# Optimization experiments

Hardware: AMD Instinct MI355X
Metric: run time of the kernel (lower is better)

The kernel has to match this reference:

```python
import jax, jax.numpy as jnp
import numpy as np
import math

D_MODEL = 1024
N_HEADS = 16
FACTOR = 5


def setup_inputs() -> dict:
    key = jax.random.key(0)
    ks = jax.random.split(key, 8)
    B, L, S, d = 8, 4096, 4096, D_MODEL
    sc = 1.0 / math.sqrt(d)
    perm = jnp.asarray(np.random.default_rng(0).permutation(L), jnp.int32)
    return {
        "queries": jax.random.normal(ks[0], (B, L, d), jnp.float32),
        "keys": jax.random.normal(ks[1], (B, S, d), jnp.float32),
        "values": jax.random.normal(ks[2], (B, S, d), jnp.float32),
        "perm": perm,
        "Wq": jax.random.normal(ks[3], (d, d), jnp.float32) * sc,
        "bq": jnp.zeros((d,), jnp.float32),
        "Wk": jax.random.normal(ks[4], (d, d), jnp.float32) * sc,
        "bk": jnp.zeros((d,), jnp.float32),
        "Wv": jax.random.normal(ks[5], (d, d), jnp.float32) * sc,
        "bv": jnp.zeros((d,), jnp.float32),
        "Wo": jax.random.normal(ks[6], (d, d), jnp.float32) * sc,
        "bo": jnp.zeros((d,), jnp.float32),
    }


def reference(queries, keys, values, perm, Wq, bq, Wk, bk, Wv, bv, Wo, bo):
    B, L, d = queries.shape
    S = keys.shape[1]
    H = N_HEADS
    dk = d // H

    q = (queries @ Wq + bq).reshape(B, L, H, dk)
    k = (keys @ Wk + bk).reshape(B, S, H, dk)
    v = (values @ Wv + bv).reshape(B, S, H, dk)

    # ProbSparse: u = min(factor * ceil(log(S)), L)  (static, shape-derived)
    u_part = FACTOR * int(math.ceil(math.log(S)))
    u = min(u_part, L)

    # sample u queries (perm replaces torch.randperm for determinism)
    q_sample = q[:, perm[:u]]                                   # [B,u,H,dk]
    scores_sample = jnp.einsum('buhd,bshd->bhus', q_sample, k)  # [B,H,u,S]

    # sparsity measurement M = max_s - mean_s
    M = scores_sample.max(-1) - scores_sample.sum(-1) / S       # [B,H,u]
    _, M_top = jax.lax.top_k(M, u)                              # [B,H,u] indices in [0,u)

    # gather top-u queries per (batch, head) along the L axis
    qT = q.transpose(0, 2, 1, 3)                                # [B,H,L,dk]
    q_red = jnp.take_along_axis(qT, M_top[..., None], axis=2)   # [B,H,u,dk]

    scores = jnp.einsum('bhud,bshd->bhus', q_red, k)            # [B,H,u,S]
    attn = jax.nn.softmax(scores, axis=-1)
    context = jnp.einsum('bhus,bshd->buhd', attn, v).reshape(B, u, d)
    output = context @ Wo + bo                                  # [B,u,d]
    return output, attn
```

## Files before the change

kernel.cpp:

```cpp
#include <hip/hip_runtime.h>
#include <stdint.h>
#include <stddef.h>

#define DEV static __device__ __forceinline__

typedef short short8 __attribute__((ext_vector_type(8)));
typedef short short4v __attribute__((ext_vector_type(4)));
typedef float f32x4 __attribute__((ext_vector_type(4)));
typedef _Float16 half8 __attribute__((ext_vector_type(8)));

DEV uint16_t f2h(float x){
  union { _Float16 h; uint16_t u; } c; c.h = (_Float16)x; return c.u;
}

DEV f32x4 mfma16h(short8 a, short8 b, f32x4 c){
  union { short8 s; half8 h; } ua, ub; ua.s = a; ub.s = b;
  return __builtin_amdgcn_mfma_f32_16x16x32_f16(ua.h, ub.h, c, 0, 0, 0);
}

typedef const __attribute__((address_space(1))) void* gas1;
typedef __attribute__((address_space(3))) void* las3;
DEV void async16(const void* g, void* l){
  __builtin_amdgcn_global_load_lds((gas1)g, (las3)l, 16, 0, 0);
}

DEV int swzoct(int row, int oct){ return (oct & ~7) | ((oct ^ row) & 7); }
DEV short8 lds_frag(const short* base, int row, int rowOcts, int oct){
  int o = swzoct(row, oct);
  return *(const short8*)(base + row * rowOcts * 8 + o * 8);
}
DEV void lds_store8(short* base, int row, int rowOcts, int oct, short8 v){
  int o = swzoct(row, oct);
  *(short8*)(base + row * rowOcts * 8 + o * 8) = v;
}

__global__ __launch_bounds__(256) void pa_prep_weights(
    const float* __restrict__ Wk, const float* __restrict__ Wv,
    uint16_t* WkT, uint16_t* WvT){
  int which = blockIdx.y;
  const float* W = which ? Wv : Wk;
  uint16_t* O = which ? WvT : WkT;
  int e0 = (blockIdx.x * 256 + threadIdx.x) * 4;
  #pragma unroll
  for(int c=0;c<4;c++){
    int e = e0 + c; int n = e >> 10, k = e & 1023;
    O[e] = f2h(W[(size_t)k*1024 + n]);
  }
}

__global__ __launch_bounds__(256) void pa_prep_inputs(
    const float* __restrict__ keys, const float* __restrict__ values,
    uint16_t* __restrict__ kf, uint16_t* __restrict__ vf){
  size_t e = ((size_t)blockIdx.x * 256 + threadIdx.x) * 8;
  const float* src = blockIdx.y ? values : keys;
  uint16_t* dst = blockIdx.y ? vf : kf;
  float4 u0 = *(const float4*)(src + e);
  float4 u1 = *(const float4*)(src + e + 4);
  float xs[8] = {u0.x,u0.y,u0.z,u0.w,u1.x,u1.y,u1.z,u1.w};
  short8 hv;
  #pragma unroll
  for(int c=0;c<8;c++) hv[c] = (short)f2h(xs[c]);
  *(short8*)(dst + e) = hv;
}

__global__ __launch_bounds__(256) void pa_q_stage1(
    const float* __restrict__ queries, const int* __restrict__ perm,
    const float* __restrict__ Wq, double* __restrict__ qpart){
  __shared__ alignas(16) float Alds[96*32];
  __shared__ alignas(16) float Blds[32*128];
  int ct = blockIdx.x, kc = blockIdx.y, b = blockIdx.z;
  int t = threadIdx.x;
  int tr = t >> 4, tc = t & 15;
  const float* qb = queries + (size_t)b*4096*1024;
  const float* srcA[3];
  #pragma unroll
  for(int rr=0; rr<3; rr++){
    int chunk = rr*256 + t;
    int row = chunk >> 3, c8 = chunk & 7;
    int rid = (row < 45) ? perm[row] : (row < 90 ? row - 45 : 0);
    srcA[rr] = qb + (size_t)rid*1024 + c8*4;
  }
  const float* srcB[4];
  #pragma unroll
  for(int rr=0; rr<4; rr++){
    int chunk = rr*256 + t;
    int kk = chunk >> 5, c = chunk & 31;
    srcB[rr] = Wq + (size_t)kk*1024 + ct*128 + c*4;
  }
  double acc[6][8];
  #pragma unroll
  for(int i=0;i<6;i++)
    #pragma unroll
    for(int jj=0;jj<8;jj++) acc[i][jj] = 0.0;
  int k0 = kc*128;
  for(int ks=0; ks<4; ks++){
    int kk0 = k0 + ks*32;
    #pragma unroll
    for(int rr=0; rr<3; rr++)
      async16(srcA[rr] + kk0, (char*)Alds + (rr*256 + t)*16);
    #pragma unroll
    for(int rr=0; rr<4; rr++)
      async16(srcB[rr] + (size_t)kk0*1024, (char*)Blds + (rr*256 + t)*16);
    __syncthreads();
    #pragma unroll
    for(int kk=0; kk<32; kk++){
      double av[6];
      #pragma unroll
      for(int i=0;i<6;i++) av[i] = (double)Alds[(tr*6+i)*32 + kk];
      float4 b0 = *(const float4*)(Blds + kk*128 + tc*8);
      float4 b1 = *(const float4*)(Blds + kk*128 + tc*8 + 4);
      double bv[8] = {(double)b0.x,(double)b0.y,(double)b0.z,(double)b0.w,
                      (double)b1.x,(double)b1.y,(double)b1.z,(double)b1.w};
      #pragma unroll
      for(int i=0;i<6;i++)
        #pragma unroll
        for(int jj=0;jj<8;jj++)
          acc[i][jj] += av[i]*bv[jj];
    }
    __syncthreads();
  }
  #pragma unroll
  for(int i=0;i<6;i++){
    int r = tr*6 + i;
    double* dst = qpart + (((size_t)b*96 + r)*8 + kc)*1024 + ct*128 + tc*8;
    #pragma unroll
    for(int jj=0;jj<8;jj++) dst[jj] = acc[i][jj];
  }
}

__global__ __launch_bounds__(256) void pa_q_finalize(
    const double* __restrict__ qpart, const float* __restrict__ bq,
    float* q_f32, uint16_t* q_f16){
  int slot = blockIdx.x, b = blockIdx.y;
  int j = (slot < 45) ? slot : ((slot >= 48 && slot < 93) ? (45 + slot - 48) : -1);
  #pragma unroll
  for(int c=0;c<4;c++){
    int n = threadIdx.x * 4 + c;
    float v = 0.f;
    if(j >= 0){
      const double* p = qpart + (((size_t)b*96 + j)*8)*1024 + n;
      double s = 0.0;
      #pragma unroll
      for(int kc=0;kc<8;kc++) s += p[(size_t)kc*1024];
      v = (float)(s + (double)bq[n]);
    }
    int h = n >> 6, d = n & 63;
    size_t idx = (((size_t)(b*16 + h))*96 + slot)*64 + d;
    q_f32[idx] = v;
    q_f16[idx] = f2h(v);
  }
}

template<bool TR>
__global__ __launch_bounds__(256) void pa_kv_gemm(
    const uint16_t* __restrict__ Ag, const uint16_t* __restrict__ Bg,
    const float* __restrict__ bias, uint16_t* __restrict__ out){
  __shared__ alignas(16) short Ah[128*64], Bh[128*64];
  int tid = threadIdx.x, wid = tid >> 6, lane = tid & 63;
  int bid = blockIdx.x;
  int xcd = bid & 7, slot = bid >> 3;
  int mt = xcd*32 + (slot >> 3), nt = slot & 7;
  int m0 = mt*128, n0 = nt*128;
  int rsub = lane >> 3;
  int soct = (lane & 7) ^ rsub;
  const uint16_t* a0 = Ag + (size_t)(m0 + wid*32 + rsub)*1024 + soct*8;
  const uint16_t* b0 = Bg + (size_t)(n0 + wid*32 + rsub)*1024 + soct*8;
  short* lA = Ah + wid*32*64;
  short* lB = Bh + wid*32*64;
  f32x4 acc[4][4];
  #pragma unroll
  for(int i=0;i<4;i++)
    #pragma unroll
    for(int jj=0;jj<4;jj++) acc[i][jj] = (f32x4){0.f,0.f,0.f,0.f};
  int wr = wid >> 1, wc = wid & 1;
  for(int kb=0; kb<16; kb++){
    int ko = kb*64;
    #pragma unroll
    for(int q=0;q<4;q++){
      async16(a0 + ko + q*8*1024, lA + q*512);
      async16(b0 + ko + q*8*1024, lB + q*512);
    }
    __syncthreads();
    short8 Af[4][2];
    #pragma unroll
    for(int mf=0;mf<4;mf++)
      #pragma unroll
      for(int k2=0;k2<2;k2++){
        int row = wr*64 + mf*16 + (lane & 15);
        int oct = k2*4 + (lane >> 4);
        Af[mf][k2] = lds_frag(Ah, row, 8, oct);
      }
    #pragma unroll
    for(int nf=0;nf<4;nf++){
      short8 Bf[2];
      #pragma unroll
      for(int k2=0;k2<2;k2++){
        int row = wc*64 + nf*16 + (lane & 15);
        int oct = k2*4 + (lane >> 4);
        Bf[k2] = lds_frag(Bh, row, 8, oct);
      }
      #pragma unroll
      for(int mf=0;mf<4;mf++)
        #pragma unroll
        for(int k2=0;k2<2;k2++)
          acc[mf][nf] = mfma16h(Af[mf][k2], Bf[k2], acc[mf][nf]);
    }
    __syncthreads();
  }
  int b = m0 >> 12, s_base = m0 & 4095;
  #pragma unroll
  for(int mf=0;mf<4;mf++)
    #pragma unroll
    for(int nf=0;nf<4;nf++){
      int srow = s_base + wr*64 + mf*16 + ((lane >> 4) << 2);
      int ncol = n0 + wc*64 + nf*16 + (lane & 15);
      float bia = bias[ncol];
      int h = ncol >> 6, d = ncol & 63;
      if constexpr(!TR){
        size_t base = ((((size_t)(b*16 + h))*4096 + srow)*64 + d);
        #pragma unroll
        for(int i=0;i<4;i++)
          out[base + (size_t)i*64] = f2h(acc[mf][nf][i] + bia);
      } else {
        short4v pk;
        #pragma unroll
        for(int i=0;i<4;i++) pk[i] = (short)f2h(acc[mf][nf][i] + bia);
        *(short4v*)(out + ((((size_t)(b*16 + h))*64 + d)*4096 + srow)) = pk;
      }
    }
}

__global__ __launch_bounds__(256) void pa_p1_stats(
    const uint16_t* __restrict__ q_f16, const uint16_t* __restrict__ khg,
    float* __restrict__ stats){
  __shared__ alignas(16) short qf[96*64], kh[128*64];
  int chunk = blockIdx.x, h = blockIdx.y, b = blockIdx.z;
  int tid = threadIdx.x, wid = tid >> 6, lane = tid & 63;
  const uint16_t* qsf = q_f16 + ((size_t)(b*16 + h))*96*64;
  #pragma unroll
  for(int jj=0;jj<3;jj++){
    int oc = tid*3 + jj;
    int sl = oc >> 3, o = oc & 7;
    lds_store8(qf, sl, 8, o, *(const short8*)(qsf + sl*64 + o*8));
  }
  float t1v[3][4], t2v[3][4], t3v[3][4], ssum[3][4], mm[3][4], zz[3][4];
  int t1i[3][4], t2i[3][4], t3i[3][4];
  #pragma unroll
  for(int a=0;a<3;a++)
    #pragma unroll
    for(int i=0;i<4;i++){
      t1v[a][i]=-3e38f; t2v[a][i]=-3e38f; t3v[a][i]=-3e38f; ssum[a][i]=0.f;
      mm[a][i]=-3e38f; zz[a][i]=0.f; t1i[a][i]=0; t2i[a][i]=0; t3i[a][i]=0;
    }
  int rsub = lane >> 3, soct = (lane & 7) ^ rsub;
  const uint16_t* khb = khg + (((size_t)(b*16 + h))*4096)*64;
  __syncthreads();
  for(int st=0; st<4; st++){
    int sg0 = chunk*512 + st*128;
    #pragma unroll
    for(int q=0;q<4;q++){
      int row = wid*32 + q*8;
      async16(khb + (size_t)(sg0 + row + rsub)*64 + soct*8, kh + row*64);
    }
    __syncthreads();
    short8 Bf[2][2];
    #pragma unroll
    for(int nf=0;nf<2;nf++)
      #pragma unroll
      for(int k2=0;k2<2;k2++){
        int scol = wid*32 + nf*16 + (lane & 15);
        int oct = k2*4 + (lane >> 4);
        Bf[nf][k2] = lds_frag(kh, scol, 8, oct);
      }
    #pragma unroll
    for(int mf=0;mf<6;mf++){
      short8 af[2];
      #pragma unroll
      for(int k2=0;k2<2;k2++){
        int row = mf*16 + (lane & 15);
        int oct = k2*4 + (lane >> 4);
        af[k2] = lds_frag(qf, row, 8, oct);
      }
      f32x4 a0 = (f32x4){0.f,0.f,0.f,0.f}, a1 = a0;
      #pragma unroll
      for(int k2=0;k2<2;k2++){
        a0 = mfma16h(af[k2], Bf[0][k2], a0);
        a1 = mfma16h(af[k2], Bf[1][k2], a1);
      }
      #pragma unroll
      for(int nf=0;nf<2;nf++){
        int sgl = sg0 + wid*32 + nf*16 + (lane & 15);
        #pragma unroll
        for(int i=0;i<4;i++){
          float v = nf ? a1[i] : a0[i];
          if(mf < 3){
            ssum[mf][i] += v;
            if(v > t1v[mf][i]){
              t3v[mf][i]=t2v[mf][i]; t3i[mf][i]=t2i[mf][i];
              t2v[mf][i]=t1v[mf][i]; t2i[mf][i]=t1i[mf][i];
              t1v[mf][i]=v; t1i[mf][i]=sgl;
            } else if(v > t2v[mf][i]){
              t3v[mf][i]=t2v[mf][i]; t3i[mf][i]=t2i[mf][i];
              t2v[mf][i]=v; t2i[mf][i]=sgl;
            } else if(v > t3v[mf][i]){
              t3v[mf][i]=v; t3i[mf][i]=sgl;
            }
          } else {
            int q = mf - 3;
            float mn = fmaxf(mm[q][i], v);
            zz[q][i] = zz[q][i]*__expf(mm[q][i]-mn) + __expf(v-mn);
            mm[q][i] = mn;
          }
        }
      }
    }
    __syncthreads();
  }
  size_t sbase = (((((size_t)b*16 + h)*8 + chunk)*4 + wid)*96)*8;
  #pragma unroll
  for(int mf=0;mf<3;mf++)
    #pragma unroll
    for(int i=0;i<4;i++){
      float v1=t1v[mf][i], v2=t2v[mf][i], v3=t3v[mf][i], sm=ssum[mf][i];
      int i1=t1i[mf][i], i2=t2i[mf][i], i3=t3i[mf][i];
      #pragma unroll
      for(int msk=1; msk<16; msk<<=1){
        float w1=__shfl_xor(v1,msk,64), w2=__shfl_xor(v2,msk,64), w3=__shfl_xor(v3,msk,64);
        int j1=__shfl_xor(i1,msk,64), j2=__shfl_xor(i2,msk,64), j3=__shfl_xor(i3,msk,64);
        sm += __shfl_xor(sm,msk,64);
        if(w1 > v1){
          float tv; int ti;
          tv=v1; v1=w1; w1=tv; ti=i1; i1=j1; j1=ti;
          tv=v2; v2=w2; w2=tv; ti=i2; i2=j2; j2=ti;
          tv=v3; v3=w3; w3=tv; ti=i3; i3=j3; j3=ti;
        }
        if(w1 > v2){
          v3=v2; i3=i2; v2=w1; i2=j1;
          if(w2 > v3){ v3=w2; i3=j2; }
        } else if(w1 > v3){ v3=w1; i3=j1; }
      }
      if((lane & 15) == 0){
        int sl = mf*16 + ((lane >> 4) << 2) + i;
        float* dst = stats + sbase + (size_t)sl*8;
        dst[0]=v1; dst[1]=__int_as_float(i1); dst[2]=v2; dst[3]=__int_as_float(i2);
        dst[4]=v3; dst[5]=__int_as_float(i3); dst[6]=sm;
      }
    }
  #pragma unroll
  for(int q=0;q<3;q++)
    #pragma unroll
    for(int i=0;i<4;i++){
      float m1=mm[q][i], z1=zz[q][i];
      #pragma unroll
      for(int msk=1; msk<16; msk<<=1){
        float m2=__shfl_xor(m1,msk,64), z2=__shfl_xor(z1,msk,64);
        float mn = fmaxf(m1,m2);
        z1 = z1*__expf(m1-mn) + z2*__expf(m2-mn);
        m1 = mn;
      }
      if((lane & 15) == 0){
        int sl = 48 + q*16 + ((lane >> 4) << 2) + i;
        float* dst = stats + sbase + (size_t)sl*8;
        dst[0]=m1; dst[1]=z1;
      }
    }
}

__global__ __launch_bounds__(256) void pa_sort_mark(
    const float* __restrict__ stats,
    float* __restrict__ mzfin,
    float* __restrict__ Mv_g, float* __restrict__ Ssum_g,
    int* __restrict__ mlist_g, int* __restrict__ clist_g,
    int* __restrict__ nmark_g){
  int h = blockIdx.x, b = blockIdx.y;
  int bh = b*16 + h;
  __shared__ float Mv[48], Ssum[48];
  __shared__ int I1[48], I2[48], I3[48];
  __shared__ int order[48], mlist[48], flags[48];
  __shared__ int clist[144];
  __shared__ int nmark;
  int t = threadIdx.x;
  const float* sb = stats + (((size_t)bh)*8*4*96)*8;
  if(t < 48) flags[t] = 0;
  if(t < 48){
    float v1=-3e38f, v2=-3e38f, v3=-3e38f, sm=0.f; int i1=0, i2=0, i3=0;
    for(int c=0;c<8;c++)
      for(int w=0;w<4;w++){
        const float* p = sb + (((size_t)c*4 + w)*96 + t)*8;
        float w1=p[0], w2=p[2], w3=p[4];
        int j1=__float_as_int(p[1]), j2=__float_as_int(p[3]), j3=__float_as_int(p[5]);
        sm += p[6];
        if(w1 > v1){
          float tv; int ti;
          tv=v1; v1=w1; w1=tv; ti=i1; i1=j1; j1=ti;
          tv=v2; v2=w2; w2=tv; ti=i2; i2=j2; j2=ti;
          tv=v3; v3=w3; w3=tv; ti=i3; i3=j3; j3=ti;
        }
        if(w1 > v2){
          v3=v2; i3=i2; v2=w1; i2=j1;
          if(w2 > v3){ v3=w2; i3=j2; }
        } else if(w1 > v3){ v3=w1; i3=j1; }
      }
    Mv[t] = v1 - sm*(1.0f/4096.0f);
    I1[t]=i1; I2[t]=i2; I3[t]=i3; Ssum[t]=sm;
  }
  if(t >= 64 && t < 112){
    int i = t - 64;
    float m1=-3e38f, z1=0.f;
    for(int c=0;c<8;c++)
      for(int w=0;w<4;w++){
        const float* p = sb + (((size_t)c*4 + w)*96 + 48 + i)*8;
        float m2=p[0], z2=p[1];
        float mn = fmaxf(m1,m2);
        z1 = z1*__expf(m1-mn) + z2*__expf(m2-mn);
        m1 = mn;
      }
    mzfin[((size_t)bh*48 + i)*2 + 0] = m1;
    mzfin[((size_t)bh*48 + i)*2 + 1] = z1;
  }
  __syncthreads();
  if(t < 64){
    float v = (t < 45) ? Mv[t] : -3e38f;
    int rank = 0;
    #pragma unroll
    for(int j=0;j<45;j++){
      float vj = __shfl(v, j, 64);
      rank += (vj > v) || (vj == v && j < (int)t);
    }
    if(t < 45) order[rank] = t;
  }
  __syncthreads();
  if(t < 44){
    if(Mv[order[t]] - Mv[order[t+1]] < 0.025f){
      flags[order[t]] = 1; flags[order[t+1]] = 1;
    }
  }
  __syncthreads();
  if(t == 0){
    int cnt=0;
    for(int i=0;i<45;i++) if(flags[i]){
      clist[3*cnt]   = I1[i];
      clist[3*cnt+1] = I2[i];
      clist[3*cnt+2] = I3[i];
      mlist[cnt++]=i;
    }
    nmark = cnt;
  }
  __syncthreads();
  int nm = nmark;
  if(t < 48){
    Mv_g[(size_t)bh*48 + t] = Mv[t];
    Ssum_g[(size_t)bh*48 + t] = Ssum[t];
  }
  if(t < nm) mlist_g[(size_t)bh*48 + t] = mlist[t];
  if(t < 3*nm) clist_g[(size_t)bh*144 + t] = clist[t];
  if(t == 0) nmark_g[bh] = nm;
}

__global__ __launch_bounds__(256) void pa_refine(
    const float* __restrict__ keys, const float* __restrict__ Wk,
    const float* __restrict__ q_f32,
    const int* __restrict__ mlist_g, const int* __restrict__ clist_g,
    const int* __restrict__ nmark_g, double* __restrict__ scx_g){
  int cid = blockIdx.x, h = blockIdx.y, b = blockIdx.z;
  int bh = b*16 + h;
  int nc = nmark_g[bh]*3;
  if(cid >= nc) return;
  __shared__ double red[256];
  int t = threadIdx.x;
  int kq = t >> 6, d = t & 63;
  int sidx = clist_g[(size_t)bh*144 + cid];
  int u = mlist_g[(size_t)bh*48 + cid/3];
  const float* krow = keys + ((size_t)b*4096 + sidx)*1024;
  double acc = 0.0;
  int col = h*64 + d;
  #pragma unroll 8
  for(int k=kq*256; k<kq*256+256; k++)
    acc += (double)krow[k] * (double)Wk[(size_t)k*1024 + col];
  red[t] = acc;
  __syncthreads();
  if(t < 64){
    double kd = red[t] + red[64+t] + red[128+t] + red[192+t];
    double sp = kd * (double)q_f32[((size_t)bh*96 + u)*64 + t];
    #pragma unroll
    for(int m=1; m<64; m<<=1) sp += __shfl_xor(sp, m, 64);
    if(t == 0) scx_g[(size_t)bh*144 + cid] = sp;
  }
}

__global__ __launch_bounds__(64) void pa_final_rank(
    const float* __restrict__ Mv_g, const float* __restrict__ Ssum_g,
    const int* __restrict__ mlist_g, const int* __restrict__ nmark_g,
    const double* __restrict__ scx_g, int* __restrict__ invrk){
  int h = blockIdx.x, b = blockIdx.y;
  int bh = b*16 + h;
  __shared__ float Mv[48];
  int t = threadIdx.x;
  if(t < 48) Mv[t] = Mv_g[(size_t)bh*48 + t];
  int nm = nmark_g[bh];
  __syncthreads();
  if(t < nm){
    int u = mlist_g[(size_t)bh*48 + t];
    const double* s3 = scx_g + (size_t)bh*144 + 3*t;
    double mx = s3[0];
    if(s3[1] > mx) mx = s3[1];
    if(s3[2] > mx) mx = s3[2];
    Mv[u] = (float)mx - Ssum_g[(size_t)bh*48 + u]*(1.0f/4096.0f);
  }
  __syncthreads();
  float v = (t < 45) ? Mv[t] : -3e38f;
  int rank = 0;
  #pragma unroll
  for(int j=0;j<45;j++){
    float vj = __shfl(v, j, 64);
    rank += (vj > v) || (vj == v && j < (int)t);
  }
  if(t < 45) invrk[(size_t)bh*48 + t] = rank;
}

__global__ __launch_bounds__(256) void pa_p2_attn(
    const uint16_t* __restrict__ q_f16, const uint16_t* __restrict__ khg,
    const uint16_t* __restrict__ v_t,
    const float* __restrict__ mzfin, const int* __restrict__ invrk,
    float* __restrict__ attn_out, float* __restrict__ ctx2){
  __shared__ alignas(16) short qf[48*64];
  __shared__ alignas(16) short kh[64*64];
  __shared__ alignas(16) short vT[64*64];
  __shared__ alignas(16) short Pl[48*64];
  int chunk = blockIdx.x, h = blockIdx.y, b = blockIdx.z;
  int tid = threadIdx.x, wid = tid >> 6, lane = tid & 63;
  const uint16_t* qsf = q_f16 + (((size_t)(b*16 + h))*96 + 48)*64;
  for(int oc=tid; oc<384; oc+=256){
    int sl = oc >> 3, o = oc & 7;
    lds_store8(qf, sl, 8, o, *(const short8*)(qsf + sl*64 + o*8));
  }
  float mreg[3][4], invz[3][4];
  int rrk[3][4];
  #pragma unroll
  for(int mf=0;mf<3;mf++)
    #pragma unroll
    for(int i=0;i<4;i++){
      int u = mf*16 + ((lane >> 4) << 2) + i;
      mreg[mf][i] = mzfin[(((size_t)(b*16 + h))*48 + u)*2 + 0];
      invz[mf][i] = 1.f / mzfin[(((size_t)(b*16 + h))*48 + u)*2 + 1];
      rrk[mf][i] = invrk[((size_t)(b*16 + h))*48 + u];
    }
  f32x4 ctx[3];
  #pragma unroll
  for(int mf=0;mf<3;mf++) ctx[mf] = (f32x4){0.f,0.f,0.f,0.f};
  int rsub = lane >> 3, soct = (lane & 7) ^ rsub;
  const uint16_t* khb = khg + (((size_t)(b*16 + h))*4096)*64;
  const uint16_t* vtb = v_t + (((size_t)(b*16 + h))*64)*4096;
  __syncthreads();
  for(int st=0; st<8; st++){
    int sg0 = chunk*512 + st*64;
    #pragma unroll
    for(int q=0;q<2;q++){
      int row = wid*16 + q*8;
      async16(khb + (size_t)(sg0 + row + rsub)*64 + soct*8, kh + row*64);
      async16(vtb + (size_t)(row + rsub)*4096 + sg0 + soct*8, vT + row*64);
    }
    __syncthreads();
    short8 Bf[2];
    #pragma unroll
    for(int k2=0;k2<2;k2++){
      int scol = wid*16 + (lane & 15);
      int oct = k2*4 + (lane >> 4);
      Bf[k2] = lds_frag(kh, scol, 8, oct);
    }
    #pragma unroll
    for(int mf=0;mf<3;mf++){
      short8 af[2];
      #pragma unroll
      for(int k2=0;k2<2;k2++){
        int row = mf*16 + (lane & 15);
        int oct = k2*4 + (lane >> 4);
        af[k2] = lds_frag(qf, row, 8, oct);
      }
      f32x4 a0 = (f32x4){0.f,0.f,0.f,0.f};
      #pragma unroll
      for(int k2=0;k2<2;k2++)
        a0 = mfma16h(af[k2], Bf[k2], a0);
      int scl = wid*16 + (lane & 15);
      #pragma unroll
      for(int i=0;i<4;i++){
        int u = mf*16 + ((lane >> 4) << 2) + i;
        float p = __expf(a0[i] - mreg[mf][i]) * invz[mf][i];
        if(u < 45){
          attn_out[(((size_t)(b*16 + h))*45 + rrk[mf][i])*4096 + sg0 + scl] = p;
        }
        int oct = scl >> 3;
        int o = (oct ^ (u & 7)) & 7;
        Pl[u*64 + o*8 + (scl & 7)] = (short)f2h(p);
      }
    }
    __syncthreads();
    #pragma unroll
    for(int k2=0;k2<2;k2++){
      int oct = k2*4 + (lane >> 4);
      int drow = wid*16 + (lane & 15);
      short8 bv = lds_frag(vT, drow, 8, oct);
      #pragma unroll
      for(int mf=0;mf<3;mf++){
        int row = mf*16 + (lane & 15);
        short8 ap = lds_frag(Pl, row, 8, oct);
        ctx[mf] = mfma16h(ap, bv, ctx[mf]);
      }
    }
    __syncthreads();
  }
  #pragma unroll
  for(int mf=0;mf<3;mf++)
    #pragma unroll
    for(int i=0;i<4;i++){
      int u = mf*16 + ((lane >> 4) << 2) + i;
      if(u < 45){
        int d = wid*16 + (lane & 15);
        ctx2[(((size_t)chunk*8 + b)*45 + rrk[mf][i])*1024 + h*64 + d] = ctx[mf][i];
      }
    }
}

__global__ __launch_bounds__(256) void pa_out_gemm(
    const float* __restrict__ ctx2, const float* __restrict__ Wo,
    const float* __restrict__ bo, float* __restrict__ out){
  __shared__ float cl[8][1024];
  int bx = blockIdx.x, by = blockIdx.y;
  int t = threadIdx.x;
  for(int e=t; e<8*1024; e+=256){
    int rr = e >> 10, k = e & 1023;
    size_t grow = (size_t)by*8 + rr;
    float s = 0.f;
    #pragma unroll
    for(int c=0;c<8;c++) s += ctx2[((size_t)c*360 + grow)*1024 + k];
    cl[rr][k] = s;
  }
  __syncthreads();
  int quad = t & 63, rg = t >> 6;
  int n = bx*256 + quad*4;
  float acc[2][4];
  #pragma unroll
  for(int rr=0;rr<2;rr++)
    #pragma unroll
    for(int c=0;c<4;c++) acc[rr][c]=0.f;
  for(int k=0;k<1024;k++){
    float4 w = *(const float4*)(Wo + (size_t)k*1024 + n);
    float c0 = cl[rg*2][k], c1 = cl[rg*2+1][k];
    acc[0][0] += c0*w.x; acc[0][1] += c0*w.y; acc[0][2] += c0*w.z; acc[0][3] += c0*w.w;
    acc[1][0] += c1*w.x; acc[1][1] += c1*w.y; acc[1][2] += c1*w.z; acc[1][3] += c1*w.w;
  }
  #pragma unroll
  for(int rr=0;rr<2;rr++){
    size_t grow = (size_t)by*8 + rg*2 + rr;
    #pragma unroll
    for(int c=0;c<4;c++) out[grow*1024 + n + c] = acc[rr][c] + bo[n + c];
  }
}

extern "C" void kernel_launch(void* const* d_in, const int* in_sizes, int n_in,
                              void* d_out, int out_size, void* d_ws, size_t ws_size,
                              hipStream_t stream){
  const float* queries = (const float*)d_in[0];
  const float* keys    = (const float*)d_in[1];
  const float* values  = (const float*)d_in[2];
  const int*   perm    = (const int*)d_in[3];
  const float* Wq = (const float*)d_in[4]; const float* bq = (const float*)d_in[5];
  const float* Wk = (const float*)d_in[6]; const float* bk = (const float*)d_in[7];
  const float* Wv = (const float*)d_in[8]; const float* bv = (const float*)d_in[9];
  const float* Wo = (const float*)d_in[10]; const float* bo = (const float*)d_in[11];

  char* ws = (char*)d_ws;
  const size_t SZ = (size_t)33554432;
  uint16_t* kf_in = (uint16_t*)(ws);
  uint16_t* vf_in = (uint16_t*)(ws + SZ*2);
  uint16_t* k_o   = (uint16_t*)(ws + SZ*4);
  uint16_t* WkT   = (uint16_t*)(ws + SZ*6);
  uint16_t* WvT   = (uint16_t*)(ws + SZ*6 + 2097152);
  float*    q_f32 = (float*)   (ws + SZ*6 + 4194304);
  uint16_t* q_f16 = (uint16_t*)(ws + SZ*6 + 7340032);

  char* rg = ws + SZ*2;
  double* qpart   = (double*)rg;
  float*  stats   = (float*)rg;
  float*  mzfin   = (float*)(rg + 12582912);
  int*    invrk   = (int*)  (rg + 12632064);
  float*  ctx2    = (float*)(rg + 12656640);
  float*  Mv_g    = (float*)(rg + 24453120);
  float*  Ssum_g  = (float*)(rg + 24477696);
  int*    mlist_g = (int*)  (rg + 24502272);
  int*    clist_g = (int*)  (rg + 24526848);
  int*    nmark_g = (int*)  (rg + 24600576);
  double* scx_g   = (double*)(rg + 24601088);
  uint16_t* v_t = kf_in;

  float* out  = (float*)d_out;
  float* attn = out + (size_t)360*1024;

  pa_prep_weights<<<dim3(1024,2), 256, 0, stream>>>(Wk, Wv, WkT, WvT);
  pa_q_stage1<<<dim3(8,8,8), 256, 0, stream>>>(queries, perm, Wq, qpart);
  pa_q_finalize<<<dim3(96,8), 256, 0, stream>>>(qpart, bq, q_f32, q_f16);
  pa_prep_inputs<<<dim3(16384,2), 256, 0, stream>>>(keys, values, kf_in, vf_in);
  pa_kv_gemm<false><<<2048, 256, 0, stream>>>(kf_in, WkT, bk, k_o);
  pa_kv_gemm<true><<<2048, 256, 0, stream>>>(vf_in, WvT, bv, v_t);
  pa_p1_stats<<<dim3(8,16,8), 256, 0, stream>>>(q_f16, k_o, stats);
  pa_sort_mark<<<dim3(16,8), 256, 0, stream>>>(stats, mzfin, Mv_g, Ssum_g, mlist_g, clist_g, nmark_g);
  pa_refine<<<dim3(135,16,8), 256, 0, stream>>>(keys, Wk, q_f32, mlist_g, clist_g, nmark_g, scx_g);
  pa_final_rank<<<dim3(16,8), 64, 0, stream>>>(Mv_g, Ssum_g, mlist_g, nmark_g, scx_g, invrk);
  pa_p2_attn<<<dim3(8,16,8), 256, 0, stream>>>(q_f16, k_o, v_t, mzfin, invrk, attn, ctx2);
  pa_out_gemm<<<dim3(4,45), 256, 0, stream>>>(ctx2, Wo, bo, out);
}
```

Before: 636.8 us.

## Merge K and V projection GEMMs into one launch with 128-wide K tiles

The two templated K and V projection GEMM launches become one kernel with a 2D grid, where blockIdx.y picks K or V operands, so both projections run concurrently. The K-step tile grows from 64 to 128, halving loop iterations and barriers per block while doubling LDS use to 64 KB per block. v_t now gets its own workspace buffer instead of aliasing kf_in, which removes the write-after-read hazard between the two GEMMs but enlarges the workspace. The larger LDS footprint may lower occupancy, and the bool template becomes a runtime branch.

```diff
diff --git a/kernel.cpp b/kernel.cpp
--- a/kernel.cpp
+++ b/kernel.cpp
@@ -151,58 +151,63 @@
   }
 }
 
-template<bool TR>
 __global__ __launch_bounds__(256) void pa_kv_gemm(
-    const uint16_t* __restrict__ Ag, const uint16_t* __restrict__ Bg,
-    const float* __restrict__ bias, uint16_t* __restrict__ out){
-  __shared__ alignas(16) short Ah[128*64], Bh[128*64];
+    const uint16_t* __restrict__ kfA, const uint16_t* __restrict__ vfA,
+    const uint16_t* __restrict__ WkB, const uint16_t* __restrict__ WvB,
+    const float* __restrict__ bk, const float* __restrict__ bv,
+    uint16_t* __restrict__ k_o, uint16_t* __restrict__ v_t){
+  __shared__ alignas(16) short Ah[128*128], Bh[128*128];
+  const bool TR = (blockIdx.y == 1);
+  const uint16_t* Ag = TR ? vfA : kfA;
+  const uint16_t* Bg = TR ? WvB : WkB;
+  const float* bias = TR ? bv : bk;
   int tid = threadIdx.x, wid = tid >> 6, lane = tid & 63;
   int bid = blockIdx.x;
   int xcd = bid & 7, slot = bid >> 3;
   int mt = xcd*32 + (slot >> 3), nt = slot & 7;
   int m0 = mt*128, n0 = nt*128;
-  int rsub = lane >> 3;
-  int soct = (lane & 7) ^ rsub;
-  const uint16_t* a0 = Ag + (size_t)(m0 + wid*32 + rsub)*1024 + soct*8;
-  const uint16_t* b0 = Bg + (size_t)(n0 + wid*32 + rsub)*1024 + soct*8;
-  short* lA = Ah + wid*32*64;
-  short* lB = Bh + wid*32*64;
+  int rsub = lane >> 4;
+  int l15 = lane & 15;
+  short* lA = Ah + wid*32*128;
+  short* lB = Bh + wid*32*128;
   f32x4 acc[4][4];
   #pragma unroll
   for(int i=0;i<4;i++)
     #pragma unroll
     for(int jj=0;jj<4;jj++) acc[i][jj] = (f32x4){0.f,0.f,0.f,0.f};
   int wr = wid >> 1, wc = wid & 1;
-  for(int kb=0; kb<16; kb++){
-    int ko = kb*64;
-    #pragma unroll
-    for(int q=0;q<4;q++){
-      async16(a0 + ko + q*8*1024, lA + q*512);
-      async16(b0 + ko + q*8*1024, lB + q*512);
-    }
-    __syncthreads();
-    short8 Af[4][2];
+  for(int kb=0; kb<8; kb++){
+    int ko = kb*128;
+    #pragma unroll
+    for(int q=0;q<8;q++){
+      int row = wid*32 + q*4 + rsub;
+      int so = (l15 & 8) | ((l15 ^ row) & 7);
+      async16(Ag + (size_t)(m0 + row)*1024 + ko + so*8, lA + q*512);
+      async16(Bg + (size_t)(n0 + row)*1024 + ko + so*8, lB + q*512);
+    }
+    __syncthreads();
+    short8 Af[4][4];
     #pragma unroll
     for(int mf=0;mf<4;mf++)
       #pragma unroll
-      for(int k2=0;k2<2;k2++){
-        int row = wr*64 + mf*16 + (lane & 15);
+      for(int k2=0;k2<4;k2++){
+        int row = wr*64 + mf*16 + l15;
         int oct = k2*4 + (lane >> 4);
-        Af[mf][k2] = lds_frag(Ah, row, 8, oct);
+        Af[mf][k2] = lds_frag(Ah, row, 16, oct);
       }
     #pragma unroll
     for(int nf=0;nf<4;nf++){
-      short8 Bf[2];
-      #pragma unroll
-      for(int k2=0;k2<2;k2++){
-        int row = wc*64 + nf*16 + (lane & 15);
+      short8 Bf[4];
+      #pragma unroll
+      for(int k2=0;k2<4;k2++){
+        int row = wc*64 + nf*16 + l15;
         int oct = k2*4 + (lane >> 4);
-        Bf[k2] = lds_frag(Bh, row, 8, oct);
+        Bf[k2] = lds_frag(Bh, row, 16, oct);
       }
       #pragma unroll
       for(int mf=0;mf<4;mf++)
         #pragma unroll
-        for(int k2=0;k2<2;k2++)
+        for(int k2=0;k2<4;k2++)
           acc[mf][nf] = mfma16h(Af[mf][k2], Bf[k2], acc[mf][nf]);
     }
     __syncthreads();
@@ -213,19 +218,19 @@
     #pragma unroll
     for(int nf=0;nf<4;nf++){
       int srow = s_base + wr*64 + mf*16 + ((lane >> 4) << 2);
-      int ncol = n0 + wc*64 + nf*16 + (lane & 15);
+      int ncol = n0 + wc*64 + nf*16 + l15;
       float bia = bias[ncol];
       int h = ncol >> 6, d = ncol & 63;
-      if constexpr(!TR){
+      if(!TR){
         size_t base = ((((size_t)(b*16 + h))*4096 + srow)*64 + d);
         #pragma unroll
         for(int i=0;i<4;i++)
-          out[base + (size_t)i*64] = f2h(acc[mf][nf][i] + bia);
+          k_o[base + (size_t)i*64] = f2h(acc[mf][nf][i] + bia);
       } else {
         short4v pk;
         #pragma unroll
         for(int i=0;i<4;i++) pk[i] = (short)f2h(acc[mf][nf][i] + bia);
-        *(short4v*)(out + ((((size_t)(b*16 + h))*64 + d)*4096 + srow)) = pk;
+        *(short4v*)(v_t + ((((size_t)(b*16 + h))*64 + d)*4096 + srow)) = pk;
       }
     }
 }
@@ -674,10 +679,11 @@
   uint16_t* kf_in = (uint16_t*)(ws);
   uint16_t* vf_in = (uint16_t*)(ws + SZ*2);
   uint16_t* k_o   = (uint16_t*)(ws + SZ*4);
-  uint16_t* WkT   = (uint16_t*)(ws + SZ*6);
-  uint16_t* WvT   = (uint16_t*)(ws + SZ*6 + 2097152);
-  float*    q_f32 = (float*)   (ws + SZ*6 + 4194304);
-  uint16_t* q_f16 = (uint16_t*)(ws + SZ*6 + 7340032);
+  uint16_t* v_t   = (uint16_t*)(ws + SZ*6);
+  uint16_t* WkT   = (uint16_t*)(ws + SZ*8);
+  uint16_t* WvT   = (uint16_t*)(ws + SZ*8 + 2097152);
+  float*    q_f32 = (float*)   (ws + SZ*8 + 4194304);
+  uint16_t* q_f16 = (uint16_t*)(ws + SZ*8 + 7340032);
 
   char* rg = ws + SZ*2;
   double* qpart   = (double*)rg;
@@ -691,7 +697,6 @@
   int*    clist_g = (int*)  (rg + 24526848);
   int*    nmark_g = (int*)  (rg + 24600576);
   double* scx_g   = (double*)(rg + 24601088);
-  uint16_t* v_t = kf_in;
 
   float* out  = (float*)d_out;
   float* attn = out + (size_t)360*1024;
@@ -700,8 +705,7 @@
   pa_q_stage1<<<dim3(8,8,8), 256, 0, stream>>>(queries, perm, Wq, qpart);
   pa_q_finalize<<<dim3(96,8), 256, 0, stream>>>(qpart, bq, q_f32, q_f16);
   pa_prep_inputs<<<dim3(16384,2), 256, 0, stream>>>(keys, values, kf_in, vf_in);
-  pa_kv_gemm<false><<<2048, 256, 0, stream>>>(kf_in, WkT, bk, k_o);
-  pa_kv_gemm<true><<<2048, 256, 0, stream>>>(vf_in, WvT, bv, v_t);
+  pa_kv_gemm<<<dim3(2048,2), 256, 0, stream>>>(kf_in, vf_in, WkT, WvT, bk, bv, k_o, v_t);
   pa_p1_stats<<<dim3(8,16,8), 256, 0, stream>>>(q_f16, k_o, stats);
   pa_sort_mark<<<dim3(16,8), 256, 0, stream>>>(stats, mzfin, Mv_g, Ssum_g, mlist_g, clist_g, nmark_g);
   pa_refine<<<dim3(135,16,8), 256, 0, stream>>>(keys, Wk, q_f32, mlist_g, clist_g, nmark_g, scx_g);
```

New measurement: 647.2 us. Within noise of the previous version (+1.6%).
